# Optimization experiments

Hardware: AMD Instinct MI355X
Metric: run time of the kernel (lower is better)

The kernel has to match this reference:

```python
import jax, jax.numpy as jnp
import numpy as np

N = 262144   # active voxel sites
C = 128      # channels (inplanes == outplanes)
K = 27       # 3^3 submanifold kernel offsets
EPS = 1e-4   # scn BatchNormalization default eps


def setup_inputs() -> dict:
    key = jax.random.key(0)
    ks = jax.random.split(key, 5)
    features = jax.random.normal(ks[0], (N, C), dtype=jnp.float32)
    nbr_idx = jax.random.randint(ks[1], (N, K), 0, N, dtype=jnp.int32)
    nbr_mask = jax.random.randint(ks[2], (N, K), 0, 2, dtype=jnp.int32)
    center = K // 2  # submanifold: center offset is always the site itself
    nbr_idx = nbr_idx.at[:, center].set(jnp.arange(N, dtype=jnp.int32))
    nbr_mask = nbr_mask.at[:, center].set(1)
    s = 1.0 / np.sqrt(K * C).astype(np.float32)
    W1 = jax.random.normal(ks[3], (K, C, C), dtype=jnp.float32) * s
    W2 = jax.random.normal(ks[4], (K, C, C), dtype=jnp.float32) * s
    bias1 = jnp.zeros((C,), jnp.float32)
    bias2 = jnp.zeros((C,), jnp.float32)
    gamma1 = jnp.ones((C,), jnp.float32)
    beta1 = jnp.zeros((C,), jnp.float32)
    gamma2 = jnp.ones((C,), jnp.float32)
    beta2 = jnp.zeros((C,), jnp.float32)
    return dict(features=features, nbr_idx=nbr_idx, nbr_mask=nbr_mask,
                gamma1=gamma1, beta1=beta1, W1=W1, bias1=bias1,
                gamma2=gamma2, beta2=beta2, W2=W2, bias2=bias2)


def _bn_relu(x, gamma, beta):
    # BatchNormReLU over active sites (training-mode batch stats)
    mu = jnp.mean(x, axis=0)
    var = jnp.mean(jnp.square(x - mu), axis=0)
    scale = gamma * jax.lax.rsqrt(var + EPS)
    return jax.nn.relu((x - mu) * scale + beta)


def _subm_conv(x, nbr_idx, nbr_mask, W, b):
    # Rulebook-based submanifold conv: for each of K offsets, gather the
    # active neighbor feature (masked) and apply that offset's [Cin,Cout] matmul.
    m = nbr_mask.astype(x.dtype)
    acc = jnp.broadcast_to(b, (x.shape[0], W.shape[2]))
    for k in range(K):  # fixed small unroll over kernel offsets
        g = x[nbr_idx[:, k]] * m[:, k:k + 1]   # [N, Cin]
        acc = acc + g @ W[k]                    # [N, Cout]
    return acc


def reference(features, nbr_idx, nbr_mask, gamma1, beta1, W1, bias1,
              gamma2, beta2, W2, bias2):
    h = _bn_relu(features, gamma1, beta1)
    h = _subm_conv(h, nbr_idx, nbr_mask, W1, bias1)
    h = _bn_relu(h, gamma2, beta2)
    h = _subm_conv(h, nbr_idx, nbr_mask, W2, bias2)
    return h + features  # AddTable residual
```

## Files before the change

kernel.cpp:

```cpp
#include <hip/hip_runtime.h>

#define NS 262144
#define NK 27

typedef float f32x4 __attribute__((ext_vector_type(4)));
typedef __bf16 bf16x8 __attribute__((ext_vector_type(8)));

__device__ __forceinline__ unsigned short f2bf(float f) {
  union { float f; unsigned int i; } c; c.f = f;
  unsigned int r = c.i + 0x7fffu + ((c.i >> 16) & 1u);
  return (unsigned short)(r >> 16);
}
__device__ __forceinline__ float bf2f(unsigned short u) {
  union { unsigned int i; float f; } c; c.i = ((unsigned int)u) << 16;
  return c.f;
}
__device__ __forceinline__ void async16(const void* gp, void* lp) {
  __builtin_amdgcn_global_load_lds((const __attribute__((address_space(1))) void*)gp,
                                   (__attribute__((address_space(3))) void*)lp, 16, 0, 0);
}

__global__ __launch_bounds__(256) void prep_idx_kernel(const int* __restrict__ nidx,
                                                       const int* __restrict__ nmask,
                                                       int* __restrict__ idx2t) {
  __shared__ int li[256 * NK];
  __shared__ int lm[256 * NK];
  const int t = threadIdx.x;
  const int sb = blockIdx.x * 256;
  for (int j = t; j < 256 * NK; j += 256) {
    li[j] = nidx[(size_t)sb * NK + j];
    lm[j] = nmask[(size_t)sb * NK + j];
  }
  __syncthreads();
  for (int k = 0; k < NK; ++k) {
    int m = lm[t * NK + k];
    int v = li[t * NK + k];
    idx2t[(size_t)k * NS + sb + t] = m ? v : NS;
  }
}

__global__ __launch_bounds__(256) void prep_w_kernel(const float* __restrict__ W1,
                                                     const float* __restrict__ W2,
                                                     unsigned short* __restrict__ Wt1,
                                                     unsigned short* __restrict__ Wt2) {
  const int b = blockIdx.x;
  const float* W = (b < NK) ? W1 : W2;
  unsigned short* Wt = (b < NK) ? Wt1 : Wt2;
  const int k = (b < NK) ? b : b - NK;
  __shared__ unsigned short tile[128 * 130];
  const int t = threadIdx.x;
  for (int j = t; j < 16384; j += 256) {
    int ci = j >> 7, co = j & 127;
    tile[ci * 130 + co] = f2bf(W[(size_t)k * 16384 + j]);
  }
  __syncthreads();
  for (int j = t; j < 16384; j += 256) {
    int co = j >> 7, ci = j & 127;
    Wt[(size_t)k * 16384 + j] = tile[ci * 130 + co];
  }
}

__global__ __launch_bounds__(256) void stats_kernel(const float* __restrict__ x,
                                                    float* __restrict__ ssum,
                                                    float* __restrict__ sssq) {
  const int t = threadIdx.x;
  const int c4 = (t & 31) * 4;
  const int rsub = t >> 5;
  const int rowend = blockIdx.x * 512 + 512;
  float s0 = 0, s1 = 0, s2 = 0, s3 = 0, q0 = 0, q1 = 0, q2 = 0, q3 = 0;
  for (int r = blockIdx.x * 512 + rsub; r < rowend; r += 8) {
    const float4 v = *(const float4*)&x[(size_t)r * 128 + c4];
    s0 += v.x; q0 += v.x * v.x;
    s1 += v.y; q1 += v.y * v.y;
    s2 += v.z; q2 += v.z * v.z;
    s3 += v.w; q3 += v.w * v.w;
  }
  __shared__ float red[256 * 8];
  red[t * 8 + 0] = s0; red[t * 8 + 1] = s1; red[t * 8 + 2] = s2; red[t * 8 + 3] = s3;
  red[t * 8 + 4] = q0; red[t * 8 + 5] = q1; red[t * 8 + 6] = q2; red[t * 8 + 7] = q3;
  __syncthreads();
  if (t < 32) {
    float a0 = 0, a1 = 0, a2 = 0, a3 = 0, b0 = 0, b1 = 0, b2 = 0, b3 = 0;
    for (int j = 0; j < 8; ++j) {
      const float* p = &red[(j * 32 + t) * 8];
      a0 += p[0]; a1 += p[1]; a2 += p[2]; a3 += p[3];
      b0 += p[4]; b1 += p[5]; b2 += p[6]; b3 += p[7];
    }
    atomicAdd(&ssum[t * 4 + 0], a0); atomicAdd(&ssum[t * 4 + 1], a1);
    atomicAdd(&ssum[t * 4 + 2], a2); atomicAdd(&ssum[t * 4 + 3], a3);
    atomicAdd(&sssq[t * 4 + 0], b0); atomicAdd(&sssq[t * 4 + 1], b1);
    atomicAdd(&sssq[t * 4 + 2], b2); atomicAdd(&sssq[t * 4 + 3], b3);
  }
}

__global__ __launch_bounds__(256) void apply_f32_kernel(const float* __restrict__ x,
    const float* __restrict__ ssum, const float* __restrict__ sssq,
    const float* __restrict__ gamma, const float* __restrict__ beta,
    unsigned short* __restrict__ hout) {
  const size_t base = ((size_t)blockIdx.x * 256 + threadIdx.x) * 8;
  const int c0 = (int)(base & 127);
  const float4 v0 = *(const float4*)&x[base];
  const float4 v1 = *(const float4*)&x[base + 4];
  const float vv[8] = {v0.x, v0.y, v0.z, v0.w, v1.x, v1.y, v1.z, v1.w};
  unsigned short o[8] __attribute__((aligned(16)));
  const float invN = 1.0f / (float)NS;
  #pragma unroll
  for (int j = 0; j < 8; ++j) {
    const int c = c0 + j;
    const float mean = ssum[c] * invN;
    const float var = sssq[c] * invN - mean * mean;
    const float sc = gamma[c] * rsqrtf(var + 1e-4f);
    const float t = (vv[j] - mean) * sc + beta[c];
    o[j] = f2bf(fmaxf(t, 0.0f));
  }
  *(int4*)&hout[base] = *(const int4*)o;
  if (blockIdx.x == 0 && threadIdx.x < 16) {
    int4 z; z.x = 0; z.y = 0; z.z = 0; z.w = 0;
    ((int4*)(hout + (size_t)NS * 128))[threadIdx.x] = z;
  }
}

__global__ __launch_bounds__(256) void apply_bf16_kernel(const unsigned short* __restrict__ x,
    const float* __restrict__ ssum, const float* __restrict__ sssq,
    const float* __restrict__ gamma, const float* __restrict__ beta,
    unsigned short* __restrict__ hout) {
  const size_t base = ((size_t)blockIdx.x * 256 + threadIdx.x) * 8;
  const int c0 = (int)(base & 127);
  unsigned short in[8] __attribute__((aligned(16)));
  *(int4*)in = *(const int4*)&x[base];
  unsigned short o[8] __attribute__((aligned(16)));
  const float invN = 1.0f / (float)NS;
  #pragma unroll
  for (int j = 0; j < 8; ++j) {
    const int c = c0 + j;
    const float mean = ssum[c] * invN;
    const float var = sssq[c] * invN - mean * mean;
    const float sc = gamma[c] * rsqrtf(var + 1e-4f);
    const float t = (bf2f(in[j]) - mean) * sc + beta[c];
    o[j] = f2bf(fmaxf(t, 0.0f));
  }
  *(int4*)&hout[base] = *(const int4*)o;
}

template <bool FIRST>
__global__ __launch_bounds__(256, 3) void conv_kernel(
    const unsigned short* __restrict__ h,
    const int* __restrict__ idx2t,
    const unsigned short* __restrict__ Wt,
    const float* __restrict__ bias,
    unsigned short* __restrict__ out_bf,
    float* __restrict__ ssum, float* __restrict__ sssq,
    const float* __restrict__ resid,
    float* __restrict__ outf) {
  __shared__ unsigned short A_lds[128 * 64];
  __shared__ unsigned short B_lds[128 * 64];
  const int tid = threadIdx.x;
  const int wave = tid >> 6, lane = tid & 63;
  const int wm = wave >> 1, wn = wave & 1;
  const int i16 = lane & 15, quad = lane >> 4;
  const int lrow = lane >> 3, lch = lane & 7;
  const int sch = lch ^ lrow;
  const int sb = blockIdx.x << 7;

  f32x4 acc[4][4];
  #pragma unroll
  for (int a = 0; a < 4; ++a)
    #pragma unroll
    for (int b = 0; b < 4; ++b) { acc[a][b][0] = 0.f; acc[a][b][1] = 0.f; acc[a][b][2] = 0.f; acc[a][b][3] = 0.f; }

  for (int k = 0; k < NK; ++k) {
    int ridx[4];
    #pragma unroll
    for (int i = 0; i < 4; ++i)
      ridx[i] = idx2t[k * NS + sb + wave * 32 + i * 8 + lrow];
    #pragma unroll
    for (int half = 0; half < 2; ++half) {
      __syncthreads();
      #pragma unroll
      for (int i = 0; i < 4; ++i) {
        const unsigned short* gb =
            Wt + (((size_t)k << 14) + ((wave * 32 + i * 8 + lrow) << 7) + (half << 6) + (sch << 3));
        async16(gb, B_lds + ((wave * 4 + i) << 9));
        const unsigned short* ga =
            h + (((size_t)ridx[i]) << 7) + (half << 6) + (sch << 3);
        async16(ga, A_lds + ((wave * 4 + i) << 9));
      }
      __syncthreads();
      #pragma unroll
      for (int ks = 0; ks < 2; ++ks) {
        const int chunk = (ks * 4 + quad) ^ (i16 & 7);
        bf16x8 af[4], bfr[4];
        #pragma unroll
        for (int mi = 0; mi < 4; ++mi)
          af[mi] = *(const bf16x8*)&A_lds[((wm * 64 + mi * 16 + i16) << 6) + (chunk << 3)];
        #pragma unroll
        for (int ni = 0; ni < 4; ++ni)
          bfr[ni] = *(const bf16x8*)&B_lds[((wn * 64 + ni * 16 + i16) << 6) + (chunk << 3)];
        #pragma unroll
        for (int mi = 0; mi < 4; ++mi)
          #pragma unroll
          for (int ni = 0; ni < 4; ++ni)
            acc[mi][ni] = __builtin_amdgcn_mfma_f32_16x16x32_bf16(af[mi], bfr[ni], acc[mi][ni], 0, 0, 0);
      }
    }
  }

  if (FIRST) {
    float cs[4], cq[4];
    #pragma unroll
    for (int ni = 0; ni < 4; ++ni) {
      const int col = wn * 64 + ni * 16 + i16;
      const float bv = bias[col];
      float s = 0.f, q = 0.f;
      #pragma unroll
      for (int mi = 0; mi < 4; ++mi) {
        const int rowb = sb + wm * 64 + mi * 16 + quad * 4;
        #pragma unroll
        for (int i = 0; i < 4; ++i) {
          const float v = acc[mi][ni][i] + bv;
          out_bf[(size_t)(rowb + i) * 128 + col] = f2bf(v);
          s += v; q += v * v;
        }
      }
      cs[ni] = s; cq[ni] = q;
    }
    #pragma unroll
    for (int ni = 0; ni < 4; ++ni) {
      cs[ni] += __shfl_xor(cs[ni], 16); cs[ni] += __shfl_xor(cs[ni], 32);
      cq[ni] += __shfl_xor(cq[ni], 16); cq[ni] += __shfl_xor(cq[ni], 32);
    }
    __syncthreads();
    float* red = (float*)A_lds;
    if (wm == 1 && quad == 0) {
      #pragma unroll
      for (int ni = 0; ni < 4; ++ni) {
        const int col = wn * 64 + ni * 16 + i16;
        red[col] = cs[ni]; red[128 + col] = cq[ni];
      }
    }
    __syncthreads();
    if (wm == 0 && quad == 0) {
      #pragma unroll
      for (int ni = 0; ni < 4; ++ni) {
        const int col = wn * 64 + ni * 16 + i16;
        atomicAdd(&ssum[col], cs[ni] + red[col]);
        atomicAdd(&sssq[col], cq[ni] + red[128 + col]);
      }
    }
  } else {
    #pragma unroll
    for (int ni = 0; ni < 4; ++ni) {
      const int col = wn * 64 + ni * 16 + i16;
      const float bv = bias[col];
      #pragma unroll
      for (int mi = 0; mi < 4; ++mi) {
        const int rowb = sb + wm * 64 + mi * 16 + quad * 4;
        #pragma unroll
        for (int i = 0; i < 4; ++i) {
          const size_t o = (size_t)(rowb + i) * 128 + col;
          outf[o] = acc[mi][ni][i] + bv + resid[o];
        }
      }
    }
  }
}

extern "C" void kernel_launch(void* const* d_in, const int* in_sizes, int n_in,
                              void* d_out, int out_size, void* d_ws, size_t ws_size,
                              hipStream_t stream) {
  const float* features = (const float*)d_in[0];
  const int* nbr_idx    = (const int*)d_in[1];
  const int* nbr_mask   = (const int*)d_in[2];
  const float* gamma1   = (const float*)d_in[3];
  const float* beta1    = (const float*)d_in[4];
  const float* W1       = (const float*)d_in[5];
  const float* bias1    = (const float*)d_in[6];
  const float* gamma2   = (const float*)d_in[7];
  const float* beta2    = (const float*)d_in[8];
  const float* W2       = (const float*)d_in[9];
  const float* bias2    = (const float*)d_in[10];

  char* ws = (char*)d_ws;
  size_t off = 0;
  unsigned short* h = (unsigned short*)(ws + off); off += (size_t)(NS + 1) * 128 * 2;
  unsigned short* out1 = (unsigned short*)(ws + off); off += (size_t)NS * 128 * 2;
  int* idx2t = (int*)(ws + off); off += (size_t)NK * NS * 4;
  unsigned short* Wt1 = (unsigned short*)(ws + off); off += (size_t)NK * 128 * 128 * 2;
  unsigned short* Wt2 = (unsigned short*)(ws + off); off += (size_t)NK * 128 * 128 * 2;
  float* stats = (float*)(ws + off); off += 4 * 128 * 4;
  float* sum1 = stats, *ssq1 = stats + 128, *sum2 = stats + 256, *ssq2 = stats + 384;

  hipMemsetAsync(stats, 0, 4 * 128 * 4, stream);
  prep_idx_kernel<<<NS / 256, 256, 0, stream>>>(nbr_idx, nbr_mask, idx2t);
  prep_w_kernel<<<2 * NK, 256, 0, stream>>>(W1, W2, Wt1, Wt2);
  stats_kernel<<<NS / 512, 256, 0, stream>>>(features, sum1, ssq1);
  apply_f32_kernel<<<(NS * 128) / 2048, 256, 0, stream>>>(features, sum1, ssq1, gamma1, beta1, h);
  conv_kernel<true><<<NS / 128, 256, 0, stream>>>(h, idx2t, Wt1, bias1, out1, sum2, ssq2, nullptr, nullptr);
  apply_bf16_kernel<<<(NS * 128) / 2048, 256, 0, stream>>>(out1, sum2, ssq2, gamma2, beta2, h);
  conv_kernel<false><<<NS / 128, 256, 0, stream>>>(h, idx2t, Wt2, bias2, nullptr, nullptr, nullptr,
                                                   features, (float*)d_out);
}
```

Baseline: 855.0 us.

## Double-buffer LDS tiles in conv kernel to overlap gather loads with MFMA

Converts the conv kernel's A/B shared-memory tiles to two buffers and software-pipelines the K-loop. The next half-tile's async global-to-LDS gather is issued before computing the current one, and neighbor indices are prefetched two steps ahead. This is meant to hide gather latency behind MFMA work. In exchange LDS usage doubles and the launch-bounds occupancy hint drops from 3 to 2 blocks per CU.

Result: slower. 877.6 us (+2.6%).

```diff
diff --git a/kernel.cpp b/kernel.cpp
--- a/kernel.cpp
+++ b/kernel.cpp
@@ -142,8 +142,37 @@
   *(int4*)&hout[base] = *(const int4*)o;
 }
 
+
+#define STAGE(buf, kk, half, rr)                                                        \
+  _Pragma("unroll")                                                                     \
+  for (int i = 0; i < 4; ++i) {                                                         \
+    const unsigned short* gb = Wt + (((size_t)(kk) << 14) +                             \
+        ((wave * 32 + i * 8 + lrow) << 7) + ((half) << 6) + (sch << 3));                \
+    async16(gb, &B_lds[buf][(wave * 4 + i) << 9]);                                      \
+    const unsigned short* ga = h + (((size_t)(rr)[i]) << 7) + ((half) << 6) + (sch << 3); \
+    async16(ga, &A_lds[buf][(wave * 4 + i) << 9]);                                      \
+  }
+
+#define COMPUTE(buf)                                                                    \
+  _Pragma("unroll")                                                                     \
+  for (int ks = 0; ks < 2; ++ks) {                                                      \
+    const int chunk = (ks * 4 + quad) ^ (i16 & 7);                                      \
+    bf16x8 af[4], bfr[4];                                                               \
+    _Pragma("unroll")                                                                   \
+    for (int mi = 0; mi < 4; ++mi)                                                      \
+      af[mi] = *(const bf16x8*)&A_lds[buf][((wm * 64 + mi * 16 + i16) << 6) + (chunk << 3)]; \
+    _Pragma("unroll")                                                                   \
+    for (int ni = 0; ni < 4; ++ni)                                                      \
+      bfr[ni] = *(const bf16x8*)&B_lds[buf][((wn * 64 + ni * 16 + i16) << 6) + (chunk << 3)]; \
+    _Pragma("unroll")                                                                   \
+    for (int mi = 0; mi < 4; ++mi)                                                      \
+      _Pragma("unroll")                                                                 \
+      for (int ni = 0; ni < 4; ++ni)                                                    \
+        acc[mi][ni] = __builtin_amdgcn_mfma_f32_16x16x32_bf16(af[mi], bfr[ni], acc[mi][ni], 0, 0, 0); \
+  }
+
 template <bool FIRST>
-__global__ __launch_bounds__(256, 3) void conv_kernel(
+__global__ __launch_bounds__(256, 2) void conv_kernel(
     const unsigned short* __restrict__ h,
     const int* __restrict__ idx2t,
     const unsigned short* __restrict__ Wt,
@@ -152,8 +181,8 @@
     float* __restrict__ ssum, float* __restrict__ sssq,
     const float* __restrict__ resid,
     float* __restrict__ outf) {
-  __shared__ unsigned short A_lds[128 * 64];
-  __shared__ unsigned short B_lds[128 * 64];
+  __shared__ unsigned short A_lds[2][128 * 64];
+  __shared__ unsigned short B_lds[2][128 * 64];
   const int tid = threadIdx.x;
   const int wave = tid >> 6, lane = tid & 63;
   const int wm = wave >> 1, wn = wave & 1;
@@ -168,41 +197,33 @@
     #pragma unroll
     for (int b = 0; b < 4; ++b) { acc[a][b][0] = 0.f; acc[a][b][1] = 0.f; acc[a][b][2] = 0.f; acc[a][b][3] = 0.f; }
 
+  int rc[4], rn[4];
+  #pragma unroll
+  for (int i = 0; i < 4; ++i)
+    rc[i] = idx2t[sb + wave * 32 + i * 8 + lrow];
+  STAGE(0, 0, 0, rc);
+  #pragma unroll
+  for (int i = 0; i < 4; ++i)
+    rn[i] = idx2t[(size_t)NS + sb + wave * 32 + i * 8 + lrow];
+  __syncthreads();
+
   for (int k = 0; k < NK; ++k) {
-    int ridx[4];
-    #pragma unroll
-    for (int i = 0; i < 4; ++i)
-      ridx[i] = idx2t[k * NS + sb + wave * 32 + i * 8 + lrow];
-    #pragma unroll
-    for (int half = 0; half < 2; ++half) {
-      __syncthreads();
-      #pragma unroll
-      for (int i = 0; i < 4; ++i) {
-        const unsigned short* gb =
-            Wt + (((size_t)k << 14) + ((wave * 32 + i * 8 + lrow) << 7) + (half << 6) + (sch << 3));
-        async16(gb, B_lds + ((wave * 4 + i) << 9));
-        const unsigned short* ga =
-            h + (((size_t)ridx[i]) << 7) + (half << 6) + (sch << 3);
-        async16(ga, A_lds + ((wave * 4 + i) << 9));
-      }
-      __syncthreads();
-      #pragma unroll
-      for (int ks = 0; ks < 2; ++ks) {
-        const int chunk = (ks * 4 + quad) ^ (i16 & 7);
-        bf16x8 af[4], bfr[4];
+    STAGE(1, k, 1, rc);
+    COMPUTE(0);
+    __syncthreads();
+
+    if (k + 1 < NK) {
+      STAGE(0, k + 1, 0, rn);
+      #pragma unroll
+      for (int i = 0; i < 4; ++i) rc[i] = rn[i];
+      if (k + 2 < NK) {
         #pragma unroll
-        for (int mi = 0; mi < 4; ++mi)
-          af[mi] = *(const bf16x8*)&A_lds[((wm * 64 + mi * 16 + i16) << 6) + (chunk << 3)];
-        #pragma unroll
-        for (int ni = 0; ni < 4; ++ni)
-          bfr[ni] = *(const bf16x8*)&B_lds[((wn * 64 + ni * 16 + i16) << 6) + (chunk << 3)];
-        #pragma unroll
-        for (int mi = 0; mi < 4; ++mi)
-          #pragma unroll
-          for (int ni = 0; ni < 4; ++ni)
-            acc[mi][ni] = __builtin_amdgcn_mfma_f32_16x16x32_bf16(af[mi], bfr[ni], acc[mi][ni], 0, 0, 0);
-      }
-    }
+        for (int i = 0; i < 4; ++i)
+          rn[i] = idx2t[(size_t)(k + 2) * NS + sb + wave * 32 + i * 8 + lrow];
+      }
+    }
+    COMPUTE(1);
+    __syncthreads();
   }
 
   if (FIRST) {
```

## Triple-buffer conv LDS stages with async prefetch and manual vmcnt waits

Applied to the files above, without the earlier changes.

Reworks the conv main loop from a synchronous two-barrier load-then-compute per half K-slice into a three-stage ring of 32-channel slices. The global_load_lds copies for the next two slices stay in flight while the current one runs on MFMA, using explicit s_waitcnt vmcnt and sched barriers, and neighbour indices are prefetched one offset ahead. It also raises MFMA wave priority during compute and changes the LDS swizzle to fit the narrower slices. The goal is to hide gather latency behind matrix math. The cost is more LDS (about 48KB per block, which may limit occupancy with 3 blocks/CU) and fragile hand-counted wait values.

Result: slower. 943.6 us (+10.4%).

```diff
diff --git a/kernel.cpp b/kernel.cpp
--- a/kernel.cpp
+++ b/kernel.cpp
@@ -142,6 +142,47 @@
   *(int4*)&hout[base] = *(const int4*)o;
 }
 
+
+#define WAITV(N) asm volatile("s_waitcnt vmcnt(" #N ")" ::: "memory")
+#define SBAR() do { __builtin_amdgcn_sched_barrier(0); __builtin_amdgcn_s_barrier(); \
+                    __builtin_amdgcn_sched_barrier(0); } while (0)
+#define ROT() do { int _t = b0; b0 = b1; b1 = b2; b2 = _t; } while (0)
+
+#define LOAD_ROWS(KK, D0, D1) do {                                                   \
+    D0 = idx2t[(size_t)(KK) * NS + sb + wave * 16 + rsel];                           \
+    D1 = idx2t[(size_t)(KK) * NS + sb + 64 + wave * 16 + rsel];                      \
+  } while (0)
+
+#define STAGE_U(BS, KK, QQ, R0, R1) do {                                             \
+    const unsigned short* ga0 = h + (((size_t)(R0)) << 7) + ((QQ) << 5) + (gch << 3);\
+    async16(ga0, &A_lds[(BS) + (wave << 9)]);                                        \
+    const unsigned short* gb0 = Wt + (((size_t)(KK)) << 14) +                        \
+        ((wave * 16 + rsel) << 7) + ((QQ) << 5) + (gch << 3);                        \
+    async16(gb0, &B_lds[(BS) + (wave << 9)]);                                        \
+    const unsigned short* ga1 = h + (((size_t)(R1)) << 7) + ((QQ) << 5) + (gch << 3);\
+    async16(ga1, &A_lds[(BS) + 2048 + (wave << 9)]);                                 \
+    const unsigned short* gb1 = Wt + (((size_t)(KK)) << 14) +                        \
+        ((64 + wave * 16 + rsel) << 7) + ((QQ) << 5) + (gch << 3);                   \
+    async16(gb1, &B_lds[(BS) + 2048 + (wave << 9)]);                                 \
+  } while (0)
+
+#define COMPUTE_U(BS) do {                                                           \
+    bf16x8 af[4], bfr[4];                                                            \
+    _Pragma("unroll")                                                                \
+    for (int mi = 0; mi < 4; ++mi)                                                   \
+      af[mi] = *(const bf16x8*)&A_lds[(BS) + ((wm * 64 + mi * 16 + i16) << 5) + (slotc << 3)]; \
+    _Pragma("unroll")                                                                \
+    for (int ni = 0; ni < 4; ++ni)                                                   \
+      bfr[ni] = *(const bf16x8*)&B_lds[(BS) + ((wn * 64 + ni * 16 + i16) << 5) + (slotc << 3)]; \
+    __builtin_amdgcn_s_setprio(1);                                                   \
+    _Pragma("unroll")                                                                \
+    for (int mi = 0; mi < 4; ++mi)                                                   \
+      _Pragma("unroll")                                                              \
+      for (int ni = 0; ni < 4; ++ni)                                                 \
+        acc[mi][ni] = __builtin_amdgcn_mfma_f32_16x16x32_bf16(af[mi], bfr[ni], acc[mi][ni], 0, 0, 0); \
+    __builtin_amdgcn_s_setprio(0);                                                   \
+  } while (0)
+
 template <bool FIRST>
 __global__ __launch_bounds__(256, 3) void conv_kernel(
     const unsigned short* __restrict__ h,
@@ -152,14 +193,15 @@
     float* __restrict__ ssum, float* __restrict__ sssq,
     const float* __restrict__ resid,
     float* __restrict__ outf) {
-  __shared__ unsigned short A_lds[128 * 64];
-  __shared__ unsigned short B_lds[128 * 64];
+  __shared__ unsigned short A_lds[3 * 4096];
+  __shared__ unsigned short B_lds[3 * 4096];
   const int tid = threadIdx.x;
   const int wave = tid >> 6, lane = tid & 63;
   const int wm = wave >> 1, wn = wave & 1;
   const int i16 = lane & 15, quad = lane >> 4;
-  const int lrow = lane >> 3, lch = lane & 7;
-  const int sch = lch ^ lrow;
+  const int rsel = lane >> 2;
+  const int gch = (lane & 3) ^ ((lane >> 3) & 3);
+  const int slotc = quad ^ ((i16 >> 1) & 3);
   const int sb = blockIdx.x << 7;
 
   f32x4 acc[4][4];
@@ -168,42 +210,32 @@
     #pragma unroll
     for (int b = 0; b < 4; ++b) { acc[a][b][0] = 0.f; acc[a][b][1] = 0.f; acc[a][b][2] = 0.f; acc[a][b][3] = 0.f; }
 
-  for (int k = 0; k < NK; ++k) {
-    int ridx[4];
-    #pragma unroll
-    for (int i = 0; i < 4; ++i)
-      ridx[i] = idx2t[k * NS + sb + wave * 32 + i * 8 + lrow];
-    #pragma unroll
-    for (int half = 0; half < 2; ++half) {
-      __syncthreads();
-      #pragma unroll
-      for (int i = 0; i < 4; ++i) {
-        const unsigned short* gb =
-            Wt + (((size_t)k << 14) + ((wave * 32 + i * 8 + lrow) << 7) + (half << 6) + (sch << 3));
-        async16(gb, B_lds + ((wave * 4 + i) << 9));
-        const unsigned short* ga =
-            h + (((size_t)ridx[i]) << 7) + (half << 6) + (sch << 3);
-        async16(ga, A_lds + ((wave * 4 + i) << 9));
-      }
-      __syncthreads();
-      #pragma unroll
-      for (int ks = 0; ks < 2; ++ks) {
-        const int chunk = (ks * 4 + quad) ^ (i16 & 7);
-        bf16x8 af[4], bfr[4];
-        #pragma unroll
-        for (int mi = 0; mi < 4; ++mi)
-          af[mi] = *(const bf16x8*)&A_lds[((wm * 64 + mi * 16 + i16) << 6) + (chunk << 3)];
-        #pragma unroll
-        for (int ni = 0; ni < 4; ++ni)
-          bfr[ni] = *(const bf16x8*)&B_lds[((wn * 64 + ni * 16 + i16) << 6) + (chunk << 3)];
-        #pragma unroll
-        for (int mi = 0; mi < 4; ++mi)
-          #pragma unroll
-          for (int ni = 0; ni < 4; ++ni)
-            acc[mi][ni] = __builtin_amdgcn_mfma_f32_16x16x32_bf16(af[mi], bfr[ni], acc[mi][ni], 0, 0, 0);
-      }
-    }
-  }
+  int rE0, rE1, rO0, rO1;
+  LOAD_ROWS(0, rE0, rE1);
+  LOAD_ROWS(1, rO0, rO1);
+  int b0 = 0, b1 = 4096, b2 = 8192;
+  STAGE_U(0, 0, 0, rE0, rE1);
+  STAGE_U(4096, 0, 1, rE0, rE1);
+
+  #pragma unroll 1
+  for (int kk = 0; kk < 26; kk += 2) {
+    STAGE_U(b2, kk, 2, rE0, rE1);                       WAITV(8);  SBAR(); COMPUTE_U(b0); SBAR(); ROT();
+    STAGE_U(b2, kk, 3, rE0, rE1); LOAD_ROWS(kk + 2, rE0, rE1);
+                                                        WAITV(10); SBAR(); COMPUTE_U(b0); SBAR(); ROT();
+    STAGE_U(b2, kk + 1, 0, rO0, rO1);                   WAITV(10); SBAR(); COMPUTE_U(b0); SBAR(); ROT();
+    STAGE_U(b2, kk + 1, 1, rO0, rO1);                   WAITV(8);  SBAR(); COMPUTE_U(b0); SBAR(); ROT();
+
+    STAGE_U(b2, kk + 1, 2, rO0, rO1);                   WAITV(8);  SBAR(); COMPUTE_U(b0); SBAR(); ROT();
+    { const int k3 = (kk + 3 > 26) ? 26 : kk + 3;
+      STAGE_U(b2, kk + 1, 3, rO0, rO1); LOAD_ROWS(k3, rO0, rO1); }
+                                                        WAITV(10); SBAR(); COMPUTE_U(b0); SBAR(); ROT();
+    STAGE_U(b2, kk + 2, 0, rE0, rE1);                   WAITV(10); SBAR(); COMPUTE_U(b0); SBAR(); ROT();
+    STAGE_U(b2, kk + 2, 1, rE0, rE1);                   WAITV(8);  SBAR(); COMPUTE_U(b0); SBAR(); ROT();
+  }
+  STAGE_U(b2, 26, 2, rE0, rE1);                         WAITV(8);  SBAR(); COMPUTE_U(b0); SBAR(); ROT();
+  STAGE_U(b2, 26, 3, rE0, rE1);                         WAITV(8);  SBAR(); COMPUTE_U(b0); SBAR(); ROT();
+                                                        WAITV(4);  SBAR(); COMPUTE_U(b0); SBAR(); ROT();
+                                                        WAITV(0);  SBAR(); COMPUTE_U(b0); SBAR();
 
   if (FIRST) {
     float cs[4], cq[4];
```

## Load conv operands directly from global into registers, bypassing LDS staging

Applied to the files above, without the earlier changes.

Removes the LDS staging of gathered activation rows and weight tiles. Each wave now loads its MFMA fragments straight from global memory into registers, prefetches the next offset's neighbor indices, and raises wave priority around the MFMA block. This drops the block-wide barriers and the LDS traffic. In exchange, rows and weights shared across waves are now loaded redundantly from global/L2, roughly doubling fetch traffic, and the 16-byte per-lane loads become less coalesced.

After: 1.764 ms. 106% more time.

```diff
diff --git a/kernel.cpp b/kernel.cpp
--- a/kernel.cpp
+++ b/kernel.cpp
@@ -14,10 +14,6 @@
 __device__ __forceinline__ float bf2f(unsigned short u) {
   union { unsigned int i; float f; } c; c.i = ((unsigned int)u) << 16;
   return c.f;
-}
-__device__ __forceinline__ void async16(const void* gp, void* lp) {
-  __builtin_amdgcn_global_load_lds((const __attribute__((address_space(1))) void*)gp,
-                                   (__attribute__((address_space(3))) void*)lp, 16, 0, 0);
 }
 
 __global__ __launch_bounds__(256) void prep_idx_kernel(const int* __restrict__ nidx,
@@ -152,14 +148,11 @@
     float* __restrict__ ssum, float* __restrict__ sssq,
     const float* __restrict__ resid,
     float* __restrict__ outf) {
-  __shared__ unsigned short A_lds[128 * 64];
-  __shared__ unsigned short B_lds[128 * 64];
+  __shared__ float red[256];
   const int tid = threadIdx.x;
   const int wave = tid >> 6, lane = tid & 63;
   const int wm = wave >> 1, wn = wave & 1;
   const int i16 = lane & 15, quad = lane >> 4;
-  const int lrow = lane >> 3, lch = lane & 7;
-  const int sch = lch ^ lrow;
   const int sb = blockIdx.x << 7;
 
   f32x4 acc[4][4];
@@ -168,40 +161,43 @@
     #pragma unroll
     for (int b = 0; b < 4; ++b) { acc[a][b][0] = 0.f; acc[a][b][1] = 0.f; acc[a][b][2] = 0.f; acc[a][b][3] = 0.f; }
 
+  const int cB0 = ((wn * 64 + i16) << 7) + (quad << 3);
+  const int cB1 = cB0 + (16 << 7);
+  const int cB2 = cB0 + (32 << 7);
+  const int cB3 = cB0 + (48 << 7);
+
+  const int* pI = idx2t + sb + wm * 64 + i16;
+  int r0 = pI[0], r1 = pI[16], r2 = pI[32], r3 = pI[48];
+
+  #pragma unroll 1
   for (int k = 0; k < NK; ++k) {
-    int ridx[4];
-    #pragma unroll
-    for (int i = 0; i < 4; ++i)
-      ridx[i] = idx2t[k * NS + sb + wave * 32 + i * 8 + lrow];
-    #pragma unroll
-    for (int half = 0; half < 2; ++half) {
-      __syncthreads();
-      #pragma unroll
-      for (int i = 0; i < 4; ++i) {
-        const unsigned short* gb =
-            Wt + (((size_t)k << 14) + ((wave * 32 + i * 8 + lrow) << 7) + (half << 6) + (sch << 3));
-        async16(gb, B_lds + ((wave * 4 + i) << 9));
-        const unsigned short* ga =
-            h + (((size_t)ridx[i]) << 7) + (half << 6) + (sch << 3);
-        async16(ga, A_lds + ((wave * 4 + i) << 9));
-      }
-      __syncthreads();
-      #pragma unroll
-      for (int ks = 0; ks < 2; ++ks) {
-        const int chunk = (ks * 4 + quad) ^ (i16 & 7);
-        bf16x8 af[4], bfr[4];
-        #pragma unroll
-        for (int mi = 0; mi < 4; ++mi)
-          af[mi] = *(const bf16x8*)&A_lds[((wm * 64 + mi * 16 + i16) << 6) + (chunk << 3)];
+    const unsigned short* a0 = h + (((size_t)r0) << 7) + (quad << 3);
+    const unsigned short* a1 = h + (((size_t)r1) << 7) + (quad << 3);
+    const unsigned short* a2 = h + (((size_t)r2) << 7) + (quad << 3);
+    const unsigned short* a3 = h + (((size_t)r3) << 7) + (quad << 3);
+    const unsigned short* bK = Wt + ((size_t)k << 14);
+    if (k + 1 < NK) {
+      const int* pIn = pI + (size_t)(k + 1) * NS;
+      r0 = pIn[0]; r1 = pIn[16]; r2 = pIn[32]; r3 = pIn[48];
+    }
+    #pragma unroll
+    for (int s = 0; s < 4; ++s) {
+      bf16x8 af[4], bfr[4];
+      af[0] = *(const bf16x8*)(a0 + s * 32);
+      af[1] = *(const bf16x8*)(a1 + s * 32);
+      af[2] = *(const bf16x8*)(a2 + s * 32);
+      af[3] = *(const bf16x8*)(a3 + s * 32);
+      bfr[0] = *(const bf16x8*)(bK + cB0 + s * 32);
+      bfr[1] = *(const bf16x8*)(bK + cB1 + s * 32);
+      bfr[2] = *(const bf16x8*)(bK + cB2 + s * 32);
+      bfr[3] = *(const bf16x8*)(bK + cB3 + s * 32);
+      __builtin_amdgcn_s_setprio(1);
+      #pragma unroll
+      for (int mi = 0; mi < 4; ++mi)
         #pragma unroll
         for (int ni = 0; ni < 4; ++ni)
-          bfr[ni] = *(const bf16x8*)&B_lds[((wn * 64 + ni * 16 + i16) << 6) + (chunk << 3)];
-        #pragma unroll
-        for (int mi = 0; mi < 4; ++mi)
-          #pragma unroll
-          for (int ni = 0; ni < 4; ++ni)
-            acc[mi][ni] = __builtin_amdgcn_mfma_f32_16x16x32_bf16(af[mi], bfr[ni], acc[mi][ni], 0, 0, 0);
-      }
+          acc[mi][ni] = __builtin_amdgcn_mfma_f32_16x16x32_bf16(af[mi], bfr[ni], acc[mi][ni], 0, 0, 0);
+      __builtin_amdgcn_s_setprio(0);
     }
   }
 
@@ -230,7 +226,6 @@
       cq[ni] += __shfl_xor(cq[ni], 16); cq[ni] += __shfl_xor(cq[ni], 32);
     }
     __syncthreads();
-    float* red = (float*)A_lds;
     if (wm == 1 && quad == 0) {
       #pragma unroll
       for (int ni = 0; ni < 4; ++ni) {
```
